# Performance work log

Measured on AMD Instinct MI355X. Metric: run time of the kernel, lower is better.

## Reference

```python
import jax, jax.numpy as jnp
import numpy as np

M, K1, N1, N2, N3 = 131072, 256, 1024, 1024, 256


def setup_inputs() -> dict:
    key = jax.random.key(0)
    k_x, k1, k2, k3 = jax.random.split(key, 4)
    x = jax.random.normal(k_x, (M, K1), dtype=jnp.float32)
    # Kaiming-ish scaling so softplus stays in a sane range
    w1 = jax.random.normal(k1, (K1, N1), dtype=jnp.float32) * (1.0 / np.sqrt(K1))
    w2 = jax.random.normal(k2, (N1, N2), dtype=jnp.float32) * (1.0 / np.sqrt(N1))
    w3 = jax.random.normal(k3, (N2, N3), dtype=jnp.float32) * (1.0 / np.sqrt(N2))
    return {"x": x, "w1": w1, "w2": w2, "w3": w3}


def reference(x, w1, w2, w3):
    # Fused 3-layer MLP: out = softplus(softplus(x @ W1) @ W2) @ W3
    h1 = jax.nn.softplus(x @ w1)   # [M, N1]
    h2 = jax.nn.softplus(h1 @ w2)  # [M, N2]
    return h2 @ w3                 # [M, N3]
```

## Files before the change

### kernel.cpp

```cpp
#include <hip/hip_runtime.h>

typedef __attribute__((ext_vector_type(8))) short short8;
typedef __attribute__((ext_vector_type(4))) float floatx4;
typedef __attribute__((ext_vector_type(2))) unsigned int uintx2;
typedef __attribute__((ext_vector_type(4))) unsigned int uintx4;
typedef unsigned short u16;

#define MFMA(a, b, c) __builtin_amdgcn_mfma_f32_16x16x32_bf16((a), (b), (c), 0, 0, 0)
#define BAR() do { asm volatile("" ::: "memory"); __builtin_amdgcn_s_barrier(); \
                   asm volatile("" ::: "memory"); } while (0)
#define LGKM0() asm volatile("s_waitcnt lgkmcnt(0)" ::: "memory")
#define LGKM8() asm volatile("s_waitcnt lgkmcnt(8)" ::: "memory")

__device__ __forceinline__ u16 f2bf(float f) {
  unsigned int u = __builtin_bit_cast(unsigned int, f);
  u += ((u >> 16) & 1u) + 0x7fffu;
  return (u16)(u >> 16);
}

__device__ __forceinline__ float softplus_f(float v) {
  float a = __builtin_fabsf(v);
  float e = __expf(-a);
  float l = __logf(1.0f + e);
  return __builtin_fmaxf(v, 0.0f) + l;
}

__device__ __forceinline__ unsigned int pack_sp(float lo, float hi) {
  return (unsigned int)f2bf(softplus_f(lo)) | ((unsigned int)f2bf(softplus_f(hi)) << 16);
}

__global__ void transpose_cvt(const float* __restrict__ in, u16* __restrict__ out, int K, int N) {
  __shared__ float tile[32][33];
  const int bn = blockIdx.x * 32, bk = blockIdx.y * 32;
  const int tx = threadIdx.x, ty = threadIdx.y;
#pragma unroll
  for (int i = 0; i < 32; i += 8)
    tile[ty + i][tx] = in[(size_t)(bk + ty + i) * N + bn + tx];
  __syncthreads();
#pragma unroll
  for (int i = 0; i < 32; i += 8)
    out[(size_t)(bn + ty + i) * K + bk + tx] = f2bf(tile[tx][ty + i]);
}

__device__ __forceinline__ void gld16(const void* g, void* l) {
  __builtin_amdgcn_global_load_lds((const __attribute__((address_space(1))) void*)g,
                                   (__attribute__((address_space(3))) void*)l, 16, 0, 0);
}

template <int LN>
__device__ __forceinline__ void vwait() {
  if constexpr (LN == 0) asm volatile("s_waitcnt vmcnt(0)" ::: "memory");
  else if constexpr (LN == 4) asm volatile("s_waitcnt vmcnt(4)" ::: "memory");
  else if constexpr (LN == 8) asm volatile("s_waitcnt vmcnt(8)" ::: "memory");
}

template <int K, int EPI, bool ACTF32>
__global__ __launch_bounds__(256, 2) void gemm64(const void* __restrict__ actv,
                                                 const u16* __restrict__ wt,
                                                 void* __restrict__ Cout, int N, int nbn) {
  constexpr int H = K / 64;
  constexpr int BUF = 16384;
  __shared__ u16 lds[2 * BUF];
  u16* L = lds;
  const int tid = threadIdx.x, lane = tid & 63, wv = tid >> 6;
  const int l15 = lane & 15, g = lane >> 4;
  const int wvm = wv >> 1, wvn = wv & 1;
  const int nwg = gridDim.x, o = blockIdx.x;
  const int sw = (o & 7) * (nwg >> 3) + (o >> 3);
  const int bm = sw / nbn, bn = sw % nbn;
  const size_t am0 = (size_t)bm * 128;
  const size_t wn0 = (size_t)bn * 128;

  int afo[4], wfo[4];
#pragma unroll
  for (int mt = 0; mt < 4; ++mt) {
    const int r = wvm * 64 + mt * 16 + l15;
    afo[mt] = (r * 8 + (g ^ (r & 7))) * 8;
  }
#pragma unroll
  for (int nt = 0; nt < 4; ++nt) {
    const int r = wvn * 64 + nt * 16 + l15;
    wfo[nt] = 8192 + (r * 8 + (g ^ (r & 7))) * 8;
  }

  int rS[4], qS[4];
#pragma unroll
  for (int j = 0; j < 4; ++j) {
    const int s = j * 256 + tid;
    rS[j] = s >> 3;
    qS[j] = (s & 7) ^ (rS[j] & 7);
  }
  const u16* asrc = nullptr;
  const float* fsrc = nullptr;
  if constexpr (ACTF32) fsrc = (const float*)actv + am0 * K;
  else asrc = (const u16*)actv + am0 * K;
  const u16* wsrc = wt + wn0 * K;

#define STG_W(hh)                                                                   \
  { _Pragma("unroll") for (int j = 0; j < 4; ++j)                                   \
      gld16(wsrc + (size_t)rS[j] * K + qS[j] * 8 + (hh) * 64,                       \
            L + ((hh) & 1) * BUF + 8192 + (j * 256 + tid) * 8); }
#define STG_AB(hh)                                                                  \
  { _Pragma("unroll") for (int j = 0; j < 4; ++j)                                   \
      gld16(asrc + (size_t)rS[j] * K + qS[j] * 8 + (hh) * 64,                       \
            L + ((hh) & 1) * BUF + (j * 256 + tid) * 8); }
#define STG_AF(hh)                                                                  \
  { floatx4 v0[4], v1[4];                                                           \
    _Pragma("unroll") for (int j = 0; j < 4; ++j) {                                 \
      const float* p_ = fsrc + (size_t)rS[j] * K + qS[j] * 8 + (hh) * 64;           \
      v0[j] = *(const floatx4*)p_;                                                  \
      v1[j] = *(const floatx4*)(p_ + 4);                                            \
    }                                                                               \
    _Pragma("unroll") for (int j = 0; j < 4; ++j) {                                 \
      uintx4 w_;                                                                    \
      w_.x = (unsigned)f2bf(v0[j].x) | ((unsigned)f2bf(v0[j].y) << 16);             \
      w_.y = (unsigned)f2bf(v0[j].z) | ((unsigned)f2bf(v0[j].w) << 16);             \
      w_.z = (unsigned)f2bf(v1[j].x) | ((unsigned)f2bf(v1[j].y) << 16);             \
      w_.w = (unsigned)f2bf(v1[j].z) | ((unsigned)f2bf(v1[j].w) << 16);             \
      *(uintx4*)(L + ((hh) & 1) * BUF + (j * 256 + tid) * 8) = w_;                  \
    } }

  floatx4 acc[4][4];
  const floatx4 z4 = {0.f, 0.f, 0.f, 0.f};
#pragma unroll
  for (int nt = 0; nt < 4; ++nt)
#pragma unroll
    for (int mt = 0; mt < 4; ++mt) acc[nt][mt] = z4;

  if constexpr (ACTF32) { STG_W(0) STG_AF(0) }
  else { STG_AB(0) STG_W(0) }

#pragma unroll 1
  for (int h = 0; h < H; ++h) {
    const int cb = (h & 1) * BUF;
    if (h + 1 < H) {
      if constexpr (ACTF32) { STG_W(h + 1) STG_AF(h + 1) LGKM0(); vwait<4>(); }
      else { STG_AB(h + 1) STG_W(h + 1) vwait<8>(); }
    } else {
      if constexpr (ACTF32) LGKM0();
      vwait<0>();
    }
    BAR();
    short8 a0 = *(const short8*)(L + cb + afo[0]);
    short8 a1 = *(const short8*)(L + cb + afo[1]);
    short8 a2 = *(const short8*)(L + cb + afo[2]);
    short8 a3 = *(const short8*)(L + cb + afo[3]);
    short8 w0 = *(const short8*)(L + cb + wfo[0]);
    short8 w1 = *(const short8*)(L + cb + wfo[1]);
    short8 w2 = *(const short8*)(L + cb + wfo[2]);
    short8 w3 = *(const short8*)(L + cb + wfo[3]);
    short8 b0 = *(const short8*)(L + cb + (afo[0] ^ 32));
    short8 b1 = *(const short8*)(L + cb + (afo[1] ^ 32));
    short8 b2 = *(const short8*)(L + cb + (afo[2] ^ 32));
    short8 b3 = *(const short8*)(L + cb + (afo[3] ^ 32));
    short8 x0 = *(const short8*)(L + cb + (wfo[0] ^ 32));
    short8 x1 = *(const short8*)(L + cb + (wfo[1] ^ 32));
    short8 x2 = *(const short8*)(L + cb + (wfo[2] ^ 32));
    short8 x3 = *(const short8*)(L + cb + (wfo[3] ^ 32));
    LGKM8();
    __builtin_amdgcn_s_setprio(1);
    acc[0][0] = MFMA(w0, a0, acc[0][0]);
    acc[0][1] = MFMA(w0, a1, acc[0][1]);
    acc[0][2] = MFMA(w0, a2, acc[0][2]);
    acc[0][3] = MFMA(w0, a3, acc[0][3]);
    acc[1][0] = MFMA(w1, a0, acc[1][0]);
    acc[1][1] = MFMA(w1, a1, acc[1][1]);
    acc[1][2] = MFMA(w1, a2, acc[1][2]);
    acc[1][3] = MFMA(w1, a3, acc[1][3]);
    acc[2][0] = MFMA(w2, a0, acc[2][0]);
    acc[2][1] = MFMA(w2, a1, acc[2][1]);
    acc[2][2] = MFMA(w2, a2, acc[2][2]);
    acc[2][3] = MFMA(w2, a3, acc[2][3]);
    acc[3][0] = MFMA(w3, a0, acc[3][0]);
    acc[3][1] = MFMA(w3, a1, acc[3][1]);
    acc[3][2] = MFMA(w3, a2, acc[3][2]);
    acc[3][3] = MFMA(w3, a3, acc[3][3]);
    LGKM0();
    acc[0][0] = MFMA(x0, b0, acc[0][0]);
    acc[0][1] = MFMA(x0, b1, acc[0][1]);
    acc[0][2] = MFMA(x0, b2, acc[0][2]);
    acc[0][3] = MFMA(x0, b3, acc[0][3]);
    acc[1][0] = MFMA(x1, b0, acc[1][0]);
    acc[1][1] = MFMA(x1, b1, acc[1][1]);
    acc[1][2] = MFMA(x1, b2, acc[1][2]);
    acc[1][3] = MFMA(x1, b3, acc[1][3]);
    acc[2][0] = MFMA(x2, b0, acc[2][0]);
    acc[2][1] = MFMA(x2, b1, acc[2][1]);
    acc[2][2] = MFMA(x2, b2, acc[2][2]);
    acc[2][3] = MFMA(x2, b3, acc[2][3]);
    acc[3][0] = MFMA(x3, b0, acc[3][0]);
    acc[3][1] = MFMA(x3, b1, acc[3][1]);
    acc[3][2] = MFMA(x3, b2, acc[3][2]);
    acc[3][3] = MFMA(x3, b3, acc[3][3]);
    __builtin_amdgcn_s_setprio(0);
    BAR();
  }
#undef STG_W
#undef STG_AB
#undef STG_AF

  __syncthreads();

  if constexpr (EPI == 0) {
    u16* cl = L;
#pragma unroll
    for (int nt = 0; nt < 4; ++nt)
#pragma unroll
      for (int mt = 0; mt < 4; ++mt) {
        const int m = wvm * 64 + mt * 16 + l15;
        const int n0 = wvn * 64 + nt * 16 + g * 4;
        const int j = n0 >> 3, hh = (n0 >> 2) & 1;
        uintx2 pk;
        pk.x = pack_sp(acc[nt][mt].x, acc[nt][mt].y);
        pk.y = pack_sp(acc[nt][mt].z, acc[nt][mt].w);
        *(uintx2*)(cl + m * 128 + ((j ^ (m & 7)) << 3) + (hh << 2)) = pk;
      }
    __syncthreads();
    u16* outp = (u16*)Cout;
#pragma unroll
    for (int i = 0; i < 8; ++i) {
      const int c = i * 256 + tid;
      const int m = c >> 4, j = c & 15;
      uintx4 v = *(const uintx4*)(cl + m * 128 + ((j ^ (m & 7)) << 3));
      *(uintx4*)(outp + (am0 + m) * N + wn0 + j * 8) = v;
    }
  } else {
    float* cf = (float*)L;
#pragma unroll
    for (int q = 0; q < 2; ++q) {
      if (q) __syncthreads();
      if (wvm == q) {
#pragma unroll
        for (int nt = 0; nt < 4; ++nt)
#pragma unroll
          for (int mt = 0; mt < 4; ++mt) {
            const int m = mt * 16 + l15;
            const int p = (wvn * 64 + nt * 16 + g * 4) >> 1;
            *(floatx4*)(cf + m * 128 + ((p ^ ((m & 7) << 1)) << 1)) = acc[nt][mt];
          }
      }
      __syncthreads();
      float* outp = (float*)Cout;
#pragma unroll
      for (int i = 0; i < 8; ++i) {
        const int c = i * 256 + tid;
        const int m = c >> 5, cc = c & 31;
        const int p = cc * 2;
        floatx4 v = *(const floatx4*)(cf + m * 128 + ((p ^ ((m & 7) << 1)) << 1));
        *(floatx4*)(outp + (am0 + q * 64 + m) * N + wn0 + cc * 4) = v;
      }
    }
  }
}

__global__ __launch_bounds__(512, 2) void mlp3_fused(const float* __restrict__ x,
                                                     const u16* __restrict__ w1t,
                                                     const u16* __restrict__ w2t,
                                                     const u16* __restrict__ w3t,
                                                     float* __restrict__ out) {
  __shared__ u16 h1s[64 * 1024];
  __shared__ u16 xs[64 * 256];
  const int tid = threadIdx.x, lane = tid & 63, wv = tid >> 6;
  const int l15 = lane & 15, g = lane >> 4;
  const size_t m0 = (size_t)blockIdx.x * 64;
  const floatx4 z4 = {0.f, 0.f, 0.f, 0.f};
  {
    const float* xp = x + m0 * 256;
#pragma unroll
    for (int r = 0; r < 8; ++r) {
      int idx4 = r * 512 + tid;
      int m = idx4 >> 6, k = (idx4 & 63) << 2;
      floatx4 v = *(const floatx4*)(xp + m * 256 + k);
      uintx2 pk;
      pk.x = (unsigned)f2bf(v.x) | ((unsigned)f2bf(v.y) << 16);
      pk.y = (unsigned)f2bf(v.z) | ((unsigned)f2bf(v.w) << 16);
      *(uintx2*)(xs + ((m * 256 + k) ^ ((m & 7) << 3))) = pk;
    }
  }
  __syncthreads();
#pragma unroll 1
  for (int c = 0; c < 4; ++c) {
    floatx4 acc[2][4];
#pragma unroll
    for (int t = 0; t < 2; ++t)
#pragma unroll
      for (int mt = 0; mt < 4; ++mt) acc[t][mt] = z4;
    const u16* p0 = w1t + (size_t)(c * 256 + wv * 32 + l15) * 256;
#pragma unroll
    for (int ks = 0; ks < 8; ++ks) {
      const int k = ks * 32 + g * 8;
      short8 a0 = *(const short8*)(p0 + k);
      short8 a1 = *(const short8*)(p0 + 16 * 256 + k);
      short8 b0 = *(const short8*)(xs + (((0 * 16 + l15) * 256 + k) ^ ((l15 & 7) << 3)));
      short8 b1 = *(const short8*)(xs + (((1 * 16 + l15) * 256 + k) ^ ((l15 & 7) << 3)));
      short8 b2 = *(const short8*)(xs + (((2 * 16 + l15) * 256 + k) ^ ((l15 & 7) << 3)));
      short8 b3 = *(const short8*)(xs + (((3 * 16 + l15) * 256 + k) ^ ((l15 & 7) << 3)));
      acc[0][0] = MFMA(a0, b0, acc[0][0]); acc[0][1] = MFMA(a0, b1, acc[0][1]);
      acc[0][2] = MFMA(a0, b2, acc[0][2]); acc[0][3] = MFMA(a0, b3, acc[0][3]);
      acc[1][0] = MFMA(a1, b0, acc[1][0]); acc[1][1] = MFMA(a1, b1, acc[1][1]);
      acc[1][2] = MFMA(a1, b2, acc[1][2]); acc[1][3] = MFMA(a1, b3, acc[1][3]);
    }
#pragma unroll
    for (int t = 0; t < 2; ++t)
#pragma unroll
      for (int mt = 0; mt < 4; ++mt) {
        const int n1 = c * 256 + wv * 32 + t * 16 + g * 4;
        const int m = mt * 16 + l15;
        uintx2 pk;
        pk.x = pack_sp(acc[t][mt].x, acc[t][mt].y);
        pk.y = pack_sp(acc[t][mt].z, acc[t][mt].w);
        *(uintx2*)(h1s + ((m * 1024 + n1) ^ ((m & 7) << 3))) = pk;
      }
  }
  __syncthreads();
  floatx4 acc3[2][4];
#pragma unroll
  for (int t = 0; t < 2; ++t)
#pragma unroll
    for (int mt = 0; mt < 4; ++mt) acc3[t][mt] = z4;
#pragma unroll 1
  for (int c2 = 0; c2 < 4; ++c2) {
    floatx4 acc2[2][4];
#pragma unroll
    for (int t = 0; t < 2; ++t)
#pragma unroll
      for (int mt = 0; mt < 4; ++mt) acc2[t][mt] = z4;
    {
      const u16* p0 = w2t + (size_t)(c2 * 256 + wv * 32 + l15) * 1024;
#pragma unroll 4
      for (int ks = 0; ks < 32; ++ks) {
        const int k = ks * 32 + g * 8;
        short8 a0 = *(const short8*)(p0 + k);
        short8 a1 = *(const short8*)(p0 + 16 * 1024 + k);
        short8 b0 = *(const short8*)(h1s + (((0 * 16 + l15) * 1024 + k) ^ ((l15 & 7) << 3)));
        short8 b1 = *(const short8*)(h1s + (((1 * 16 + l15) * 1024 + k) ^ ((l15 & 7) << 3)));
        short8 b2 = *(const short8*)(h1s + (((2 * 16 + l15) * 1024 + k) ^ ((l15 & 7) << 3)));
        short8 b3 = *(const short8*)(h1s + (((3 * 16 + l15) * 1024 + k) ^ ((l15 & 7) << 3)));
        acc2[0][0] = MFMA(a0, b0, acc2[0][0]); acc2[0][1] = MFMA(a0, b1, acc2[0][1]);
        acc2[0][2] = MFMA(a0, b2, acc2[0][2]); acc2[0][3] = MFMA(a0, b3, acc2[0][3]);
        acc2[1][0] = MFMA(a1, b0, acc2[1][0]); acc2[1][1] = MFMA(a1, b1, acc2[1][1]);
        acc2[1][2] = MFMA(a1, b2, acc2[1][2]); acc2[1][3] = MFMA(a1, b3, acc2[1][3]);
      }
    }
    __syncthreads();
#pragma unroll
    for (int t = 0; t < 2; ++t)
#pragma unroll
      for (int mt = 0; mt < 4; ++mt) {
        const int n2l = wv * 32 + t * 16 + g * 4;
        const int m = mt * 16 + l15;
        uintx2 pk;
        pk.x = pack_sp(acc2[t][mt].x, acc2[t][mt].y);
        pk.y = pack_sp(acc2[t][mt].z, acc2[t][mt].w);
        *(uintx2*)(xs + ((m * 256 + n2l) ^ ((m & 7) << 3))) = pk;
      }
    __syncthreads();
    {
      const u16* p0 = w3t + (size_t)(wv * 32 + l15) * 1024 + c2 * 256;
#pragma unroll
      for (int ks = 0; ks < 8; ++ks) {
        const int k = ks * 32 + g * 8;
        short8 a0 = *(const short8*)(p0 + k);
        short8 a1 = *(const short8*)(p0 + 16 * 1024 + k);
        short8 b0 = *(const short8*)(xs + (((0 * 16 + l15) * 256 + k) ^ ((l15 & 7) << 3)));
        short8 b1 = *(const short8*)(xs + (((1 * 16 + l15) * 256 + k) ^ ((l15 & 7) << 3)));
        short8 b2 = *(const short8*)(xs + (((2 * 16 + l15) * 256 + k) ^ ((l15 & 7) << 3)));
        short8 b3 = *(const short8*)(xs + (((3 * 16 + l15) * 256 + k) ^ ((l15 & 7) << 3)));
        acc3[0][0] = MFMA(a0, b0, acc3[0][0]); acc3[0][1] = MFMA(a0, b1, acc3[0][1]);
        acc3[0][2] = MFMA(a0, b2, acc3[0][2]); acc3[0][3] = MFMA(a0, b3, acc3[0][3]);
        acc3[1][0] = MFMA(a1, b0, acc3[1][0]); acc3[1][1] = MFMA(a1, b1, acc3[1][1]);
        acc3[1][2] = MFMA(a1, b2, acc3[1][2]); acc3[1][3] = MFMA(a1, b3, acc3[1][3]);
      }
    }
  }
#pragma unroll
  for (int t = 0; t < 2; ++t)
#pragma unroll
    for (int mt = 0; mt < 4; ++mt) {
      const int n3 = wv * 32 + t * 16 + g * 4;
      const int m = mt * 16 + l15;
      *(floatx4*)(out + (m0 + m) * 256 + n3) = acc3[t][mt];
    }
}

extern "C" void kernel_launch(void* const* d_in, const int* in_sizes, int n_in,
                              void* d_out, int out_size, void* d_ws, size_t ws_size,
                              hipStream_t stream) {
  const float* x = (const float*)d_in[0];
  const float* w1 = (const float*)d_in[1];
  const float* w2 = (const float*)d_in[2];
  const float* w3 = (const float*)d_in[3];
  float* out = (float*)d_out;
  const size_t M = 131072;

  u16* w1t = (u16*)d_ws;
  u16* w2t = w1t + 1024 * 256;
  u16* w3t = w2t + 1024 * 1024;
  u16* bufA = w3t + 256 * 1024;
  const size_t weights_el = 1024 * 256 + 1024 * 1024 + 256 * 1024;

  size_t CM = 0;
  const size_t cands[4] = {32768, 16384, 8192, 4096};
  for (int i = 0; i < 4; ++i) {
    size_t need = (weights_el + 2 * cands[i] * 1024) * sizeof(u16);
    if (ws_size >= need) { CM = cands[i]; break; }
  }

  dim3 tb(32, 8);
  transpose_cvt<<<dim3(32, 8), tb, 0, stream>>>(w1, w1t, 256, 1024);
  transpose_cvt<<<dim3(32, 32), tb, 0, stream>>>(w2, w2t, 1024, 1024);
  transpose_cvt<<<dim3(8, 32), tb, 0, stream>>>(w3, w3t, 1024, 256);

  if (CM) {
    u16* bufB = bufA + CM * 1024;
    const int nchunk = (int)(M / CM);
    for (int ci = 0; ci < nchunk; ++ci) {
      const float* xc = x + (size_t)ci * CM * 256;
      float* oc = out + (size_t)ci * CM * 256;
      gemm64<256, 0, true><<<(int)(CM / 128) * 8, 256, 0, stream>>>(xc, w1t, bufA, 1024, 8);
      gemm64<1024, 0, false><<<(int)(CM / 128) * 8, 256, 0, stream>>>(bufA, w2t, bufB, 1024, 8);
      gemm64<1024, 1, false><<<(int)(CM / 128) * 2, 256, 0, stream>>>(bufB, w3t, oc, 256, 2);
    }
  } else {
    mlp3_fused<<<M / 64, 512, 0, stream>>>(x, w1t, w2t, w3t, out);
  }
}
```

Baseline: 661.1 us.

## Make GEMM workgroups process multiple M tiles persistently with in-loop epilogue

Turns the tiled GEMM kernel into a semi-persistent variant where each workgroup walks NT consecutive 128-row M tiles in one continuous pipelined loop. The epilogue runs inside the loop after each tile's K sweep, and the accumulators are reset before the next tile. Layers 1 and 2 use NT=4 when the workspace allows 32K-row chunks, which cuts the grid size by four and removes per-block launch, prologue and pipeline-drain costs. The trade-off is extra barriers per tile, since the epilogue reuses the LDS buffer. With NT=4 the grid is 512 workgroups, which may underfill the GPU.

```diff
diff --git a/kernel.cpp b/kernel.cpp
--- a/kernel.cpp
+++ b/kernel.cpp
@@ -54,11 +54,14 @@
   else if constexpr (LN == 8) asm volatile("s_waitcnt vmcnt(8)" ::: "memory");
 }
 
-template <int K, int EPI, bool ACTF32>
-__global__ __launch_bounds__(256, 2) void gemm64(const void* __restrict__ actv,
-                                                 const u16* __restrict__ wt,
-                                                 void* __restrict__ Cout, int N, int nbn) {
+template <int K, int EPI, bool ACTF32, int NT>
+__global__ __launch_bounds__(256, 2) void gemmp(const void* __restrict__ actv,
+                                                const u16* __restrict__ wt,
+                                                void* __restrict__ Cout, int N, int nbn) {
   constexpr int H = K / 64;
+  constexpr int LOG2H = (H == 4 ? 2 : 4);
+  static_assert(H == 4 || H == 16, "H must be 4 or 16");
+  constexpr int NW = NT * H;
   constexpr int BUF = 16384;
   __shared__ u16 lds[2 * BUF];
   u16* L = lds;
@@ -67,8 +70,7 @@
   const int wvm = wv >> 1, wvn = wv & 1;
   const int nwg = gridDim.x, o = blockIdx.x;
   const int sw = (o & 7) * (nwg >> 3) + (o >> 3);
-  const int bm = sw / nbn, bn = sw % nbn;
-  const size_t am0 = (size_t)bm * 128;
+  const int bm0 = (sw / nbn) * NT, bn = sw % nbn;
   const size_t wn0 = (size_t)bn * 128;
 
   int afo[4], wfo[4];
@@ -92,22 +94,27 @@
   }
   const u16* asrc = nullptr;
   const float* fsrc = nullptr;
-  if constexpr (ACTF32) fsrc = (const float*)actv + am0 * K;
-  else asrc = (const u16*)actv + am0 * K;
+  if constexpr (ACTF32) fsrc = (const float*)actv + (size_t)bm0 * 128 * K;
+  else asrc = (const u16*)actv + (size_t)bm0 * 128 * K;
   const u16* wsrc = wt + wn0 * K;
 
-#define STG_W(hh)                                                                   \
-  { _Pragma("unroll") for (int j = 0; j < 4; ++j)                                   \
-      gld16(wsrc + (size_t)rS[j] * K + qS[j] * 8 + (hh) * 64,                       \
-            L + ((hh) & 1) * BUF + 8192 + (j * 256 + tid) * 8); }
-#define STG_AB(hh)                                                                  \
-  { _Pragma("unroll") for (int j = 0; j < 4; ++j)                                   \
-      gld16(asrc + (size_t)rS[j] * K + qS[j] * 8 + (hh) * 64,                       \
-            L + ((hh) & 1) * BUF + (j * 256 + tid) * 8); }
-#define STG_AF(hh)                                                                  \
-  { floatx4 v0[4], v1[4];                                                           \
+#define STG_W(uu)                                                                   \
+  { const int h_ = (uu) & (H - 1);                                                  \
+    _Pragma("unroll") for (int j = 0; j < 4; ++j)                                   \
+      gld16(wsrc + (size_t)rS[j] * K + qS[j] * 8 + h_ * 64,                         \
+            L + ((uu) & 1) * BUF + 8192 + (j * 256 + tid) * 8); }
+#define STG_AB(uu)                                                                  \
+  { const int h_ = (uu) & (H - 1);                                                  \
+    const size_t tb_ = (size_t)((uu) >> LOG2H) * 128 * K;                           \
+    _Pragma("unroll") for (int j = 0; j < 4; ++j)                                   \
+      gld16(asrc + tb_ + (size_t)rS[j] * K + qS[j] * 8 + h_ * 64,                   \
+            L + ((uu) & 1) * BUF + (j * 256 + tid) * 8); }
+#define STG_AF(uu)                                                                  \
+  { const int h_ = (uu) & (H - 1);                                                  \
+    const size_t tb_ = (size_t)((uu) >> LOG2H) * 128 * K;                           \
+    floatx4 v0[4], v1[4];                                                           \
     _Pragma("unroll") for (int j = 0; j < 4; ++j) {                                 \
-      const float* p_ = fsrc + (size_t)rS[j] * K + qS[j] * 8 + (hh) * 64;           \
+      const float* p_ = fsrc + tb_ + (size_t)rS[j] * K + qS[j] * 8 + h_ * 64;       \
       v0[j] = *(const floatx4*)p_;                                                  \
       v1[j] = *(const floatx4*)(p_ + 4);                                            \
     }                                                                               \
@@ -117,7 +124,7 @@
       w_.y = (unsigned)f2bf(v0[j].z) | ((unsigned)f2bf(v0[j].w) << 16);             \
       w_.z = (unsigned)f2bf(v1[j].x) | ((unsigned)f2bf(v1[j].y) << 16);             \
       w_.w = (unsigned)f2bf(v1[j].z) | ((unsigned)f2bf(v1[j].w) << 16);             \
-      *(uintx4*)(L + ((hh) & 1) * BUF + (j * 256 + tid) * 8) = w_;                  \
+      *(uintx4*)(L + ((uu) & 1) * BUF + (j * 256 + tid) * 8) = w_;                  \
     } }
 
   floatx4 acc[4][4];
@@ -131,11 +138,11 @@
   else { STG_AB(0) STG_W(0) }
 
 #pragma unroll 1
-  for (int h = 0; h < H; ++h) {
-    const int cb = (h & 1) * BUF;
-    if (h + 1 < H) {
-      if constexpr (ACTF32) { STG_W(h + 1) STG_AF(h + 1) LGKM0(); vwait<4>(); }
-      else { STG_AB(h + 1) STG_W(h + 1) vwait<8>(); }
+  for (int u = 0; u < NW; ++u) {
+    const int cb = (u & 1) * BUF;
+    if (u + 1 < NW) {
+      if constexpr (ACTF32) { STG_W(u + 1) STG_AF(u + 1) LGKM0(); vwait<4>(); }
+      else { STG_AB(u + 1) STG_W(u + 1) vwait<8>(); }
     } else {
       if constexpr (ACTF32) LGKM0();
       vwait<0>();
@@ -194,63 +201,73 @@
     acc[3][3] = MFMA(x3, b3, acc[3][3]);
     __builtin_amdgcn_s_setprio(0);
     BAR();
+
+    if ((u & (H - 1)) == H - 1) {
+      const size_t am0 = (size_t)(bm0 + (u >> LOG2H)) * 128;
+      u16* scr = L + cb;
+      if constexpr (EPI == 0) {
+        u16* cl = scr;
+#pragma unroll
+        for (int nt = 0; nt < 4; ++nt)
+#pragma unroll
+          for (int mt = 0; mt < 4; ++mt) {
+            const int m = wvm * 64 + mt * 16 + l15;
+            const int n0 = wvn * 64 + nt * 16 + g * 4;
+            const int j = n0 >> 3, hh = (n0 >> 2) & 1;
+            uintx2 pk;
+            pk.x = pack_sp(acc[nt][mt].x, acc[nt][mt].y);
+            pk.y = pack_sp(acc[nt][mt].z, acc[nt][mt].w);
+            *(uintx2*)(cl + m * 128 + ((j ^ (m & 7)) << 3) + (hh << 2)) = pk;
+          }
+        __syncthreads();
+        u16* outp = (u16*)Cout;
+#pragma unroll
+        for (int i = 0; i < 8; ++i) {
+          const int c = i * 256 + tid;
+          const int m = c >> 4, j = c & 15;
+          uintx4 v = *(const uintx4*)(cl + m * 128 + ((j ^ (m & 7)) << 3));
+          *(uintx4*)(outp + (am0 + m) * N + wn0 + j * 8) = v;
+        }
+        __syncthreads();
+      } else {
+        float* cf = (float*)scr;
+#pragma unroll
+        for (int q = 0; q < 2; ++q) {
+          if (q) __syncthreads();
+          if (wvm == q) {
+#pragma unroll
+            for (int nt = 0; nt < 4; ++nt)
+#pragma unroll
+              for (int mt = 0; mt < 4; ++mt) {
+                const int m = mt * 16 + l15;
+                const int p = (wvn * 64 + nt * 16 + g * 4) >> 1;
+                *(floatx4*)(cf + m * 128 + ((p ^ ((m & 7) << 1)) << 1)) = acc[nt][mt];
+              }
+          }
+          __syncthreads();
+          float* outp = (float*)Cout;
+#pragma unroll
+          for (int i = 0; i < 8; ++i) {
+            const int c = i * 256 + tid;
+            const int m = c >> 5, cc = c & 31;
+            const int p = cc * 2;
+            floatx4 v = *(const floatx4*)(cf + m * 128 + ((p ^ ((m & 7) << 1)) << 1));
+            *(floatx4*)(outp + (am0 + q * 64 + m) * N + wn0 + cc * 4) = v;
+          }
+        }
+        __syncthreads();
+      }
+      if (u + 1 < NW) {
+#pragma unroll
+        for (int nt = 0; nt < 4; ++nt)
+#pragma unroll
+          for (int mt = 0; mt < 4; ++mt) acc[nt][mt] = z4;
+      }
+    }
   }
 #undef STG_W
 #undef STG_AB
 #undef STG_AF
-
-  __syncthreads();
-
-  if constexpr (EPI == 0) {
-    u16* cl = L;
-#pragma unroll
-    for (int nt = 0; nt < 4; ++nt)
-#pragma unroll
-      for (int mt = 0; mt < 4; ++mt) {
-        const int m = wvm * 64 + mt * 16 + l15;
-        const int n0 = wvn * 64 + nt * 16 + g * 4;
-        const int j = n0 >> 3, hh = (n0 >> 2) & 1;
-        uintx2 pk;
-        pk.x = pack_sp(acc[nt][mt].x, acc[nt][mt].y);
-        pk.y = pack_sp(acc[nt][mt].z, acc[nt][mt].w);
-        *(uintx2*)(cl + m * 128 + ((j ^ (m & 7)) << 3) + (hh << 2)) = pk;
-      }
-    __syncthreads();
-    u16* outp = (u16*)Cout;
-#pragma unroll
-    for (int i = 0; i < 8; ++i) {
-      const int c = i * 256 + tid;
-      const int m = c >> 4, j = c & 15;
-      uintx4 v = *(const uintx4*)(cl + m * 128 + ((j ^ (m & 7)) << 3));
-      *(uintx4*)(outp + (am0 + m) * N + wn0 + j * 8) = v;
-    }
-  } else {
-    float* cf = (float*)L;
-#pragma unroll
-    for (int q = 0; q < 2; ++q) {
-      if (q) __syncthreads();
-      if (wvm == q) {
-#pragma unroll
-        for (int nt = 0; nt < 4; ++nt)
-#pragma unroll
-          for (int mt = 0; mt < 4; ++mt) {
-            const int m = mt * 16 + l15;
-            const int p = (wvn * 64 + nt * 16 + g * 4) >> 1;
-            *(floatx4*)(cf + m * 128 + ((p ^ ((m & 7) << 1)) << 1)) = acc[nt][mt];
-          }
-      }
-      __syncthreads();
-      float* outp = (float*)Cout;
-#pragma unroll
-      for (int i = 0; i < 8; ++i) {
-        const int c = i * 256 + tid;
-        const int m = c >> 5, cc = c & 31;
-        const int p = cc * 2;
-        floatx4 v = *(const floatx4*)(cf + m * 128 + ((p ^ ((m & 7) << 1)) << 1));
-        *(floatx4*)(outp + (am0 + q * 64 + m) * N + wn0 + cc * 4) = v;
-      }
-    }
-  }
 }
 
 __global__ __launch_bounds__(512, 2) void mlp3_fused(const float* __restrict__ x,
@@ -411,15 +428,25 @@
   transpose_cvt<<<dim3(32, 32), tb, 0, stream>>>(w2, w2t, 1024, 1024);
   transpose_cvt<<<dim3(8, 32), tb, 0, stream>>>(w3, w3t, 1024, 256);
 
-  if (CM) {
+  if (CM >= 32768) {
     u16* bufB = bufA + CM * 1024;
     const int nchunk = (int)(M / CM);
     for (int ci = 0; ci < nchunk; ++ci) {
       const float* xc = x + (size_t)ci * CM * 256;
       float* oc = out + (size_t)ci * CM * 256;
-      gemm64<256, 0, true><<<(int)(CM / 128) * 8, 256, 0, stream>>>(xc, w1t, bufA, 1024, 8);
-      gemm64<1024, 0, false><<<(int)(CM / 128) * 8, 256, 0, stream>>>(bufA, w2t, bufB, 1024, 8);
-      gemm64<1024, 1, false><<<(int)(CM / 128) * 2, 256, 0, stream>>>(bufB, w3t, oc, 256, 2);
+      gemmp<256, 0, true, 4><<<(int)(CM / 512) * 8, 256, 0, stream>>>(xc, w1t, bufA, 1024, 8);
+      gemmp<1024, 0, false, 4><<<(int)(CM / 512) * 8, 256, 0, stream>>>(bufA, w2t, bufB, 1024, 8);
+      gemmp<1024, 1, false, 1><<<(int)(CM / 128) * 2, 256, 0, stream>>>(bufB, w3t, oc, 256, 2);
+    }
+  } else if (CM) {
+    u16* bufB = bufA + CM * 1024;
+    const int nchunk = (int)(M / CM);
+    for (int ci = 0; ci < nchunk; ++ci) {
+      const float* xc = x + (size_t)ci * CM * 256;
+      float* oc = out + (size_t)ci * CM * 256;
+      gemmp<256, 0, true, 1><<<(int)(CM / 128) * 8, 256, 0, stream>>>(xc, w1t, bufA, 1024, 8);
+      gemmp<1024, 0, false, 1><<<(int)(CM / 128) * 8, 256, 0, stream>>>(bufA, w2t, bufB, 1024, 8);
+      gemmp<1024, 1, false, 1><<<(int)(CM / 128) * 2, 256, 0, stream>>>(bufB, w3t, oc, 256, 2);
     }
   } else {
     mlp3_fused<<<M / 64, 512, 0, stream>>>(x, w1t, w2t, w3t, out);
```

After: 663.1 us. About the same (+0.3%).
